# Optimization experiments

Hardware: AMD Instinct MI355X
Metric: run time of the kernel (lower is better)

## Reference

```python
import jax, jax.numpy as jnp
import numpy as np

B, NA, NB, E = 2, 256, 256, 512
H1, H2 = 300, 100


def setup_inputs() -> dict:
    key = jax.random.key(0)
    ks = jax.random.split(key, 16)

    def n(k, shape, scale=1.0):
        return jax.random.normal(k, shape, dtype=jnp.float32) * scale

    z = lambda shape: jnp.zeros(shape, jnp.float32)
    return {
        "action_embedding": n(ks[0], (B, E, NA)),
        "anchor_embedding": n(ks[1], (B, E, NB)),
        "action_points": n(ks[2], (B, 3, NA)),
        "anchor_points": n(ks[3], (B, 3, NB)),
        # pairwise MLP kernel params: 2E -> 300 -> 100 -> 1
        "mlp_W1": n(ks[4], (2 * E, H1), (2 * E) ** -0.5),
        "mlp_b1": z((H1,)),
        "mlp_W2": n(ks[5], (H1, H2), H1 ** -0.5),
        "mlp_b2": z((H2,)),
        "mlp_W3": n(ks[6], (H2, 1), H2 ** -0.5),
        "mlp_b3": z((1,)),
        # PointNet [512,64,64,64,128,512] (1x1 convs) + Conv1d(512,1,bias=False)
        "pn_W0": n(ks[7], (64, 512), 512 ** -0.5),
        "pn_b0": z((64,)),
        "pn_W1": n(ks[8], (64, 64), 64 ** -0.5),
        "pn_b1": z((64,)),
        "pn_W2": n(ks[9], (64, 64), 64 ** -0.5),
        "pn_b2": z((64,)),
        "pn_W3": n(ks[10], (128, 64), 64 ** -0.5),
        "pn_b3": z((128,)),
        "pn_W4": n(ks[11], (512, 128), 128 ** -0.5),
        "pn_b4": z((512,)),
        "head_W": n(ks[12], (1, 512), 512 ** -0.5),
    }


def reference(action_embedding, anchor_embedding, action_points, anchor_points,
              mlp_W1, mlp_b1, mlp_W2, mlp_b2, mlp_W3, mlp_b3,
              pn_W0, pn_b0, pn_W1, pn_b1, pn_W2, pn_b2, pn_W3, pn_b3,
              pn_W4, pn_b4, head_W):
    P_A = action_points.transpose(0, 2, 1)      # (B, NA, 3)
    P_B = anchor_points.transpose(0, 2, 1)      # (B, NB, 3)
    Phi_A = action_embedding.transpose(0, 2, 1)  # (B, NA, E)
    Phi_B = anchor_embedding.transpose(0, 2, 1)  # (B, NB, E)
    Ed = Phi_A.shape[-1]

    # --- symmetric pairwise MLP kernel: softplus((mlp(cat(a,b)) + mlp(cat(b,a))) / 2) ---
    # First Linear layer is split so the O(NA*NB*2E) concat is never materialized:
    # cat(a,b) @ W1 == a @ W1[:E] + b @ W1[E:]
    W1a, W1b = mlp_W1[:Ed], mlp_W1[Ed:]

    def mlp_tail(h):  # h: (B, NA, NB, H1) pre-activation of layer 1
        h = jax.nn.relu(h)
        h = jax.nn.relu(h @ mlp_W2 + mlp_b2)
        return (h @ mlp_W3 + mlp_b3)[..., 0]  # (B, NA, NB)

    hA_a = Phi_A @ W1a  # (B, NA, H1)
    hA_b = Phi_A @ W1b
    hB_a = Phi_B @ W1a  # (B, NB, H1)
    hB_b = Phi_B @ W1b
    v1 = mlp_tail(hA_a[:, :, None, :] + hB_b[:, None, :, :] + mlp_b1)  # mlp(cat(x1,x2))
    v2 = mlp_tail(hB_a[:, None, :, :] + hA_b[:, :, None, :] + mlp_b1)  # mlp(cat(x2,x1))
    R_est = jax.nn.softplus((v1 + v2) * 0.5)  # (B, NA, NB) estimated distances

    # --- weighted multilateration (estimate_p), vectorized over (B, NA) ---
    # Linearized LS: ||p||^2 - 2 q_k^T p = r_k^2 - ||q_k||^2; subtract weighted means
    # to eliminate ||p||^2, then solve 3x3 weighted normal equations per action point.
    w = jnp.ones(P_B.shape[:2], R_est.dtype)            # (B, NB) uniform weights (last_attn=False)
    wsum = w.sum(-1, keepdims=True)                      # (B, 1)
    qbar = (w[..., None] * P_B).sum(1) / wsum            # (B, 3)
    bvec = (P_B ** 2).sum(-1)[:, None, :] - R_est ** 2   # (B, NA, NB)
    bbar = (w[:, None, :] * bvec).sum(-1) / wsum         # (B, NA)
    Amat = 2.0 * (P_B - qbar[:, None, :])                # (B, NB, 3)
    yvec = bvec - bbar[..., None]                        # (B, NA, NB)
    M = jnp.einsum('bki,bk,bkj->bij', Amat, w, Amat)     # (B, 3, 3)
    rhs = jnp.einsum('bki,bk,bak->bai', Amat, w, yvec)   # (B, NA, 3)
    P_A_B_pred = jnp.linalg.solve(M[:, None], rhs[..., None])[..., 0]  # (B, NA, 3)

    flow = (P_A_B_pred - P_A).transpose(0, 2, 1)         # (B, 3, NA)

    # --- PointNet flow-weight head (1x1 convs + ReLU, final conv no bias) ---
    x = action_embedding                                  # (B, 512, NA)
    for Wc, bc in ((pn_W0, pn_b0), (pn_W1, pn_b1), (pn_W2, pn_b2),
                   (pn_W3, pn_b3), (pn_W4, pn_b4)):
        x = jax.nn.relu(jnp.einsum('oi,bin->bon', Wc, x) + bc[None, :, None])
    weight = jnp.einsum('oi,bin->bon', head_W, x)        # (B, 1, NA)

    full_flow = jnp.concatenate([flow, weight], axis=1)  # (B, 4, NA)
    return full_flow
```

## Files before the change

### kernel.cpp

```cpp
#include <hip/hip_runtime.h>
#include <hip/hip_bf16.h>
#include <hip/hip_fp16.h>

typedef float f32x4 __attribute__((ext_vector_type(4)));
typedef float f32x16 __attribute__((ext_vector_type(16)));
typedef short s16x8 __attribute__((ext_vector_type(8)));
typedef _Float16 f16x8 __attribute__((ext_vector_type(8)));

#define OFF_EMBT   0u
#define OFF_W1T    1048576u
#define OFF_W2TSW  1662976u
#define OFF_W0BF   1740800u
#define OFF_HA     1806336u
#define OFF_R2     3051520u
#define WS_TOTAL   3575808u

__device__ __forceinline__ int pack_bf2(float a, float b) {
  __hip_bfloat162 h = __float22bfloat162_rn(make_float2(a, b));
  int r; __builtin_memcpy(&r, &h, 4); return r;
}
__device__ __forceinline__ unsigned pack_f16_2(float a, float b) {
  __half2 h = __float22half2_rn(make_float2(a, b));
  unsigned r; __builtin_memcpy(&r, &h, 4); return r;
}
__device__ __forceinline__ unsigned short bf16u(float f) {
  __hip_bfloat16 h = __float2bfloat16(f);
  unsigned short u; __builtin_memcpy(&u, &h, 2); return u;
}
__device__ __forceinline__ s16x8 i4_to_s8(int a, int b, int c, int d) {
  union { int i[4]; s16x8 s; } u;
  u.i[0] = a; u.i[1] = b; u.i[2] = c; u.i[3] = d; return u.s;
}
template<int CTRL>
__device__ __forceinline__ float dpp_add(float x) {
  int xi; __builtin_memcpy(&xi, &x, 4);
  int yi = __builtin_amdgcn_update_dpp(0, xi, CTRL, 0xf, 0xf, true);
  float y; __builtin_memcpy(&y, &yi, 4);
  return x + y;
}
__device__ __forceinline__ float swz_xor16(float x) {
  int xi; __builtin_memcpy(&xi, &x, 4);
  int yi = __builtin_amdgcn_ds_swizzle(xi, 0x401f);
  float y; __builtin_memcpy(&y, &yi, 4);
  return y;
}

__global__ __launch_bounds__(256) void ka_prep(
    const float* __restrict__ act_emb, const float* __restrict__ anc_emb,
    const float* __restrict__ W1, const float* __restrict__ W2,
    const float* __restrict__ W0pn, char* __restrict__ ws)
{
  __hip_bfloat16* embT  = (__hip_bfloat16*)(ws + OFF_EMBT);
  __hip_bfloat16* W1T   = (__hip_bfloat16*)(ws + OFF_W1T);
  unsigned short* W2Tsw = (unsigned short*)(ws + OFF_W2TSW);
  unsigned short* W0bf  = (unsigned short*)(ws + OFF_W0BF);
  __shared__ float tile[64][65];
  int blk = blockIdx.x, t = threadIdx.x;
  if (blk < 128) {
    int b = blk >> 6, emb = (blk >> 5) & 1, ntile = (blk >> 3) & 3, etile = blk & 7;
    const float* src = emb ? anc_emb : act_emb;
    int e0 = etile * 64, n0 = ntile * 64;
    int rr = t >> 6, cc = t & 63;
    #pragma unroll
    for (int it2 = 0; it2 < 16; ++it2) {
      int e_l = rr * 16 + it2;
      tile[e_l][cc] = src[(size_t)(b * 512 + e0 + e_l) * 256 + n0 + cc];
    }
    __syncthreads();
    int n_l = t >> 2, eq = t & 3;
    unsigned int* dst = (unsigned int*)(embT + ((size_t)((b * 2 + emb) * 256 + n0 + n_l)) * 512 + e0 + eq * 16);
    #pragma unroll
    for (int kk = 0; kk < 8; ++kk)
      dst[kk] = (unsigned)pack_bf2(tile[eq * 16 + 2 * kk][n_l], tile[eq * 16 + 2 * kk + 1][n_l]);
  } else if (blk < 208) {
    int id = blk - 128;
    int half = id / 40; int rem = id % 40; int et = rem / 5; int ct = rem % 5;
    int e0 = et * 64, c0 = ct * 64;
    int rr = t >> 6, cc = t & 63;
    #pragma unroll
    for (int it2 = 0; it2 < 16; ++it2) {
      int e_l = rr * 16 + it2;
      int c = c0 + cc;
      tile[e_l][cc] = (c < 300) ? W1[(size_t)(half * 512 + e0 + e_l) * 300 + c] : 0.f;
    }
    __syncthreads();
    int c_l = t >> 2, eq = t & 3;
    if (c0 + c_l < 300) {
      unsigned int* dst = (unsigned int*)(W1T + ((size_t)(half * 300 + c0 + c_l)) * 512 + e0 + eq * 16);
      #pragma unroll
      for (int kk = 0; kk < 8; ++kk)
        dst[kk] = (unsigned)pack_bf2(tile[eq * 16 + 2 * kk][c_l], tile[eq * 16 + 2 * kk + 1][c_l]);
    }
  } else if (blk < 227) {
    int idx = (blk - 208) * 256 + t;
    int lane = idx & 63; int ntks = idx >> 6; int nt = ntks & 3; int ks = ntks >> 2;
    int n = nt * 32 + (lane & 31);
    int kb = ks * 16 + (lane >> 5) * 8;
    unsigned int q[4];
    #pragma unroll
    for (int jj = 0; jj < 4; ++jj) {
      int k0 = kb + jj * 2, k1 = kb + jj * 2 + 1;
      float f0 = (n < 100 && k0 < 300) ? W2[(size_t)k0 * 100 + n] : 0.f;
      float f1 = (n < 100 && k1 < 300) ? W2[(size_t)k1 * 100 + n] : 0.f;
      q[jj] = pack_f16_2(f0, f1);
    }
    ((uint4*)W2Tsw)[idx] = make_uint4(q[0], q[1], q[2], q[3]);
  } else if (blk < 243) {
    int idx = (blk - 227) * 256 + t;
    const float* s = W0pn + (size_t)idx * 8;
    ((uint4*)W0bf)[idx] = make_uint4(
        (unsigned)pack_bf2(s[0], s[1]), (unsigned)pack_bf2(s[2], s[3]),
        (unsigned)pack_bf2(s[4], s[5]), (unsigned)pack_bf2(s[6], s[7]));
  } else {
    int idx = (blk - 243) * 256 + t;
    _Float16* ha = (_Float16*)(ws + OFF_HA);
    #pragma unroll
    for (int rr = 0; rr < 2; ++rr) {
      int row = idx * 2 + rr;
      unsigned* p = (unsigned*)(ha + (size_t)row * 304 + 300);
      p[0] = 0u; p[1] = 0u;
    }
  }
}

template<int K, int NT>
__device__ __forceinline__ void pn_layer(unsigned short* xb, const float* __restrict__ W,
                                         const float* __restrict__ bias, int wv, int l, int g)
{
  constexpr int NN = NT / 4;
  f32x4 z = {0.f, 0.f, 0.f, 0.f};
  f32x4 acc[NN];
  #pragma unroll
  for (int nn = 0; nn < NN; ++nn) acc[nn] = z;
  #pragma unroll
  for (int nn = 0; nn < NN; ++nn) {
    int o = (wv + nn * 4) * 16 + l;
    const float* wr0 = W + (size_t)o * K;
    #pragma unroll
    for (int ks = 0; ks < K / 32; ++ks) {
      int koff = ks * 32 + g * 8;
      f32x4 wa = *(const f32x4*)(wr0 + koff);
      f32x4 wb = *(const f32x4*)(wr0 + koff + 4);
      s16x8 bfr = i4_to_s8(pack_bf2(wa.x, wa.y), pack_bf2(wa.z, wa.w),
                           pack_bf2(wb.x, wb.y), pack_bf2(wb.z, wb.w));
      s16x8 a0 = *(const s16x8*)(xb + (size_t)l * 520 + koff);
      acc[nn] = __builtin_amdgcn_mfma_f32_16x16x32_bf16(a0, bfr, acc[nn], 0, 0, 0);
    }
  }
  __syncthreads();
  #pragma unroll
  for (int nn = 0; nn < NN; ++nn) {
    int chan = (wv + nn * 4) * 16 + l;
    float bv = bias[chan];
    #pragma unroll
    for (int r = 0; r < 4; ++r)
      xb[(size_t)(g * 4 + r) * 520 + chan] = bf16u(fmaxf(acc[nn][r] + bv, 0.f));
  }
  __syncthreads();
}

__global__ __launch_bounds__(256) void k1_ha(
    const __hip_bfloat16* __restrict__ embT, const __hip_bfloat16* __restrict__ W1T,
    const float* __restrict__ b1, _Float16* __restrict__ ha_ws,
    const unsigned short* __restrict__ W0bf,
    const float* __restrict__ pnW1, const float* __restrict__ pnW2,
    const float* __restrict__ pnW3, const float* __restrict__ pnW4,
    const float* __restrict__ pnB0, const float* __restrict__ pnB1,
    const float* __restrict__ pnB2, const float* __restrict__ pnB3,
    const float* __restrict__ pnB4,
    const float* __restrict__ headW, float* __restrict__ out)
{
  __shared__ unsigned short xbuf[16 * 520];
  int blk = blockIdx.x, t = threadIdx.x;
  int wv = t >> 6, lane = t & 63, l = lane & 15, g = lane >> 4;
  if (blk < 320) {
    int b = blk / 160; int r = blk % 160; int emb = r / 80; r %= 80;
    int mch = r / 5; int nch = r % 5;
    int m0 = mch * 16;
    const unsigned short* Ap = (const unsigned short*)embT +
        ((size_t)((b * 2 + emb) * 256 + m0 + l)) * 512;
    const unsigned short* Wp = (const unsigned short*)W1T;
    f32x4 z = {0.f, 0.f, 0.f, 0.f};
    f32x4 acc[2] = {z, z};
    for (int ks = 0; ks < 16; ++ks) {
      int k0 = ks * 32 + g * 8;
      s16x8 af = *(const s16x8*)(Ap + k0);
      #pragma unroll
      for (int q = 0; q < 2; ++q) {
        int c = nch * 120 + (wv * 2 + q) * 16 + l;
        s16x8 bf = {0, 0, 0, 0, 0, 0, 0, 0};
        if (c < 600) bf = *(const s16x8*)(Wp + (size_t)c * 512 + k0);
        acc[q] = __builtin_amdgcn_mfma_f32_16x16x32_bf16(af, bf, acc[q], 0, 0, 0);
      }
    }
    #pragma unroll
    for (int q = 0; q < 2; ++q) {
      int cl = (wv * 2 + q) * 16 + l;
      int c = nch * 120 + cl;
      if (cl < 120 && c < 600) {
        int half = (c >= 300) ? 1 : 0;
        int cc = c - half * 300;
        float bias = (emb == 0) ? b1[cc] : 0.f;
        _Float16* Dp = ha_ws + ((size_t)((b * 4 + emb * 2 + half) * 256 + m0 + g * 4)) * 304 + cc;
        #pragma unroll
        for (int r2 = 0; r2 < 4; ++r2)
          Dp[(size_t)r2 * 304] = (_Float16)__float2half_rn(acc[q][r2] + bias);
      }
    }
  } else {
    int pn = blk - 320;
    int b_pn = pn >> 4, n0 = (pn & 15) * 16;
    unsigned short* xb = xbuf;
    {
      const unsigned short* A0 = (const unsigned short*)embT + ((size_t)(b_pn * 2 * 256 + n0)) * 512;
      f32x4 acc0 = {0.f, 0.f, 0.f, 0.f};
      int o = wv * 16 + l;
      const unsigned short* w0r = W0bf + (size_t)o * 512;
      #pragma unroll
      for (int ks = 0; ks < 16; ++ks) {
        int koff = ks * 32 + g * 8;
        s16x8 bfr = *(const s16x8*)(w0r + koff);
        s16x8 a0 = *(const s16x8*)(A0 + (size_t)l * 512 + koff);
        acc0 = __builtin_amdgcn_mfma_f32_16x16x32_bf16(a0, bfr, acc0, 0, 0, 0);
      }
      float bv = pnB0[o];
      #pragma unroll
      for (int r2 = 0; r2 < 4; ++r2)
        xb[(size_t)(g * 4 + r2) * 520 + o] = bf16u(fmaxf(acc0[r2] + bv, 0.f));
      __syncthreads();
    }
    pn_layer<64, 4>(xb, pnW1, pnB1, wv, l, g);
    pn_layer<64, 4>(xb, pnW2, pnB2, wv, l, g);
    pn_layer<64, 8>(xb, pnW3, pnB3, wv, l, g);
    pn_layer<128, 32>(xb, pnW4, pnB4, wv, l, g);
    {
      int p_l = t >> 4, os = t & 15;
      const unsigned short* row = xb + (size_t)p_l * 520 + os * 32;
      float s = 0.f;
      #pragma unroll
      for (int c = 0; c < 32; ++c) {
        unsigned int u = ((unsigned int)row[c]) << 16;
        float xv; __builtin_memcpy(&xv, &u, 4);
        s += xv * headW[os * 32 + c];
      }
      s += __shfl_xor(s, 1); s += __shfl_xor(s, 2);
      s += __shfl_xor(s, 4); s += __shfl_xor(s, 8);
      if (os == 0) out[(size_t)(b_pn * 4 + 3) * 256 + n0 + p_l] = s;
    }
  }
}

__global__ __launch_bounds__(512, 4) void k2_main(
    const _Float16* __restrict__ ha_ws, const unsigned short* __restrict__ W2Tsw,
    const float* __restrict__ b2g, const float* __restrict__ W3g, const float* __restrict__ b3g,
    float* __restrict__ R2)
{
  __shared__ int4 w2s[4864];
  __shared__ float ex[4][2][16];
  int blk = blockIdx.x, t = threadIdx.x;
  int wv = t >> 6, lane = t & 63, col = lane & 31, hi = lane >> 5;
  int jl = wv & 3, nh = wv >> 2;
  int u = blk; int b = u >> 8; u &= 255; int it = u >> 5; int jtp = u & 31;
  int i0 = it * 32;
  int j0 = jtp * 8 + jl;
  {
    const int4* w2g = (const int4*)W2Tsw;
    #pragma unroll
    for (int q = 0; q < 9; ++q) { int idx = t + q * 512; w2s[idx] = w2g[idx]; }
    { int idx = t + 9 * 512; if (idx < 4864) w2s[idx] = w2g[idx]; }
  }
  const _Float16* pA0 = ha_ws + ((size_t)((b * 4 + 0) * 256 + i0 + col)) * 304 + hi * 8;
  const _Float16* pA1 = ha_ws + ((size_t)((b * 4 + 1) * 256 + i0 + col)) * 304 + hi * 8;
  const _Float16* pB0 = ha_ws + ((size_t)((b * 4 + 3) * 256 + j0)) * 304 + hi * 8;
  const _Float16* pB1 = ha_ws + ((size_t)((b * 4 + 2) * 256 + j0)) * 304 + hi * 8;
  f16x8 a0c = *(const f16x8*)(pA0);
  f16x8 a1c = *(const f16x8*)(pA1);
  f16x8 b0c = *(const f16x8*)(pB0);
  f16x8 b1c = *(const f16x8*)(pB1);
  __syncthreads();

  const f16x8 zf = {0, 0, 0, 0, 0, 0, 0, 0};
  const int4* wbase = &w2s[nh * 128 + lane];
  f32x16 z16;
  #pragma unroll
  for (int q = 0; q < 16; ++q) z16[q] = 0.f;

  #pragma unroll 1
  for (int s = 0; s < 2; ++s) {
    f32x16 acc00 = z16, acc01 = z16, acc10 = z16, acc11 = z16;
    #pragma unroll 1
    for (int ks = 0; ks < 19; ++ks) {
      f16x8 a0n, a1n, b0n, b1n;
      if (ks < 18) {
        int ko = (ks + 1) * 16;
        a0n = *(const f16x8*)(pA0 + ko);
        a1n = *(const f16x8*)(pA1 + ko);
        b0n = *(const f16x8*)(pB0 + s * 1216 + ko);
        b1n = *(const f16x8*)(pB1 + s * 1216 + ko);
      } else if (s == 0) {
        a0n = *(const f16x8*)(pA0);
        a1n = *(const f16x8*)(pA1);
        b0n = *(const f16x8*)(pB0 + 1216);
        b1n = *(const f16x8*)(pB1 + 1216);
      } else {
        a0n = a0c; a1n = a1c; b0n = b0c; b1n = b1c;
      }
      f16x8 af0 = __builtin_elementwise_max(a0c + b0c, zf);
      f16x8 af1 = __builtin_elementwise_max(a1c + b1c, zf);
      const int4* wp = wbase + ks * 256;
      f16x8 bf0 = *(const f16x8*)(wp);
      f16x8 bf1 = *(const f16x8*)(wp + 64);
      acc00 = __builtin_amdgcn_mfma_f32_32x32x16_f16(af0, bf0, acc00, 0, 0, 0);
      acc01 = __builtin_amdgcn_mfma_f32_32x32x16_f16(af0, bf1, acc01, 0, 0, 0);
      acc10 = __builtin_amdgcn_mfma_f32_32x32x16_f16(af1, bf0, acc10, 0, 0, 0);
      acc11 = __builtin_amdgcn_mfma_f32_32x32x16_f16(af1, bf1, acc11, 0, 0, 0);
      a0c = a0n; a1c = a1n; b0c = b0n; b1c = b1n;
    }
    int j = j0 + s * 4;
    int n0 = nh * 64 + col, n1 = n0 + 32;
    float w3v0 = (n0 < 100) ? W3g[n0] : 0.f;
    float w3v1 = (n1 < 100) ? W3g[n1] : 0.f;
    float b2v0 = (n0 < 100) ? b2g[n0] : 0.f;
    float b2v1 = (n1 < 100) ? b2g[n1] : 0.f;
    float b3 = b3g[0];
    float mine = 0.f;
    #pragma unroll
    for (int r = 0; r < 16; ++r) {
      float x = fmaxf(acc00[r] + b2v0, 0.f) * w3v0 + fmaxf(acc01[r] + b2v1, 0.f) * w3v1
              + fmaxf(acc10[r] + b2v0, 0.f) * w3v0 + fmaxf(acc11[r] + b2v1, 0.f) * w3v1;
      x = dpp_add<0xB1>(x);
      x = dpp_add<0x4E>(x);
      x = dpp_add<0x141>(x);
      x = dpp_add<0x140>(x);
      x += swz_xor16(x);
      if (col == r) mine = x;
    }
    __syncthreads();
    if (nh == 1 && col < 16) ex[jl][hi][col] = mine;
    __syncthreads();
    if (nh == 0 && col < 16) {
      float tot = mine + ex[jl][hi][col];
      float S = 0.5f * tot + b3;
      float Rr = (S > 20.f) ? S : log1pf(expf(S));
      int il = (col & 3) + 8 * (col >> 2) + 4 * hi;
      R2[((size_t)(b * 256 + i0 + il)) * 256 + j] = Rr * Rr;
    }
  }
}

__device__ __forceinline__ float block_sum(float v, float* redbuf, int t) {
  #pragma unroll
  for (int m = 1; m < 64; m <<= 1) v += __shfl_xor(v, m);
  __syncthreads();
  if ((t & 63) == 0) redbuf[t >> 6] = v;
  __syncthreads();
  return redbuf[0] + redbuf[1] + redbuf[2] + redbuf[3];
}

__global__ __launch_bounds__(256) void k3_solve(
    const float* __restrict__ anc_pts, const float* __restrict__ act_pts,
    const float* __restrict__ R2, float* __restrict__ out)
{
  __shared__ float Ax[256], Ay[256], Az[256];
  __shared__ float redbuf[4];
  int blk = blockIdx.x, t = threadIdx.x;
  int b = blk >> 2, ic = blk & 3;
  int k = t;
  float px = anc_pts[(size_t)(b * 3 + 0) * 256 + k];
  float py = anc_pts[(size_t)(b * 3 + 1) * 256 + k];
  float pz = anc_pts[(size_t)(b * 3 + 2) * 256 + k];
  float qx = block_sum(px, redbuf, t) * (1.f / 256.f);
  float qy = block_sum(py, redbuf, t) * (1.f / 256.f);
  float qz = block_sum(pz, redbuf, t) * (1.f / 256.f);
  float ax = 2.f * (px - qx), ay = 2.f * (py - qy), az = 2.f * (pz - qz);
  float p2 = px * px + py * py + pz * pz;
  Ax[k] = ax; Ay[k] = ay; Az[k] = az;
  float mxx = block_sum(ax * ax, redbuf, t);
  float mxy = block_sum(ax * ay, redbuf, t);
  float mxz = block_sum(ax * az, redbuf, t);
  float myy = block_sum(ay * ay, redbuf, t);
  float myz = block_sum(ay * az, redbuf, t);
  float mzz = block_sum(az * az, redbuf, t);
  float c0x = block_sum(ax * p2, redbuf, t);
  float c0y = block_sum(ay * p2, redbuf, t);
  float c0z = block_sum(az * p2, redbuf, t);
  __syncthreads();
  float det = mxx * (myy * mzz - myz * myz) - mxy * (mxy * mzz - myz * mxz) + mxz * (mxy * myz - myy * mxz);
  float idet = 1.f / det;
  float i00 = (myy * mzz - myz * myz) * idet;
  float i01 = (mxz * myz - mxy * mzz) * idet;
  float i02 = (mxy * myz - mxz * myy) * idet;
  float i11 = (mxx * mzz - mxz * mxz) * idet;
  float i12 = (mxy * mxz - mxx * myz) * idet;
  float i22 = (mxx * myy - mxy * mxy) * idet;
  int il = t >> 2, ks = t & 3;
  int i = ic * 64 + il;
  const float* rrow = R2 + ((size_t)(b * 256 + i)) * 256;
  float r0 = 0.f, r1 = 0.f, r2 = 0.f;
  #pragma unroll
  for (int kk = 0; kk < 16; ++kk) {
    int kb = ks * 64 + kk * 4;
    f32x4 rv = *(const f32x4*)(rrow + kb);
    r0 += Ax[kb] * rv.x + Ax[kb + 1] * rv.y + Ax[kb + 2] * rv.z + Ax[kb + 3] * rv.w;
    r1 += Ay[kb] * rv.x + Ay[kb + 1] * rv.y + Ay[kb + 2] * rv.z + Ay[kb + 3] * rv.w;
    r2 += Az[kb] * rv.x + Az[kb + 1] * rv.y + Az[kb + 2] * rv.z + Az[kb + 3] * rv.w;
  }
  r0 += __shfl_xor(r0, 1); r0 += __shfl_xor(r0, 2);
  r1 += __shfl_xor(r1, 1); r1 += __shfl_xor(r1, 2);
  r2 += __shfl_xor(r2, 1); r2 += __shfl_xor(r2, 2);
  if (ks == 0) {
    float hx = c0x - r0, hy = c0y - r1, hz = c0z - r2;
    float x0 = i00 * hx + i01 * hy + i02 * hz;
    float x1 = i01 * hx + i11 * hy + i12 * hz;
    float x2 = i02 * hx + i12 * hy + i22 * hz;
    out[(size_t)(b * 4 + 0) * 256 + i] = x0 - act_pts[(size_t)(b * 3 + 0) * 256 + i];
    out[(size_t)(b * 4 + 1) * 256 + i] = x1 - act_pts[(size_t)(b * 3 + 1) * 256 + i];
    out[(size_t)(b * 4 + 2) * 256 + i] = x2 - act_pts[(size_t)(b * 3 + 2) * 256 + i];
  }
}

extern "C" void kernel_launch(void* const* d_in, const int* in_sizes, int n_in,
                              void* d_out, int out_size, void* d_ws, size_t ws_size,
                              hipStream_t stream)
{
  const float* act_emb = (const float*)d_in[0];
  const float* anc_emb = (const float*)d_in[1];
  const float* act_pts = (const float*)d_in[2];
  const float* anc_pts = (const float*)d_in[3];
  const float* W1  = (const float*)d_in[4];
  const float* b1  = (const float*)d_in[5];
  const float* W2  = (const float*)d_in[6];
  const float* b2  = (const float*)d_in[7];
  const float* W3  = (const float*)d_in[8];
  const float* b3  = (const float*)d_in[9];
  const float* pnW0 = (const float*)d_in[10];
  const float* pnB0 = (const float*)d_in[11];
  const float* pnW1 = (const float*)d_in[12];
  const float* pnB1 = (const float*)d_in[13];
  const float* pnW2 = (const float*)d_in[14];
  const float* pnB2 = (const float*)d_in[15];
  const float* pnW3 = (const float*)d_in[16];
  const float* pnB3 = (const float*)d_in[17];
  const float* pnW4 = (const float*)d_in[18];
  const float* pnB4 = (const float*)d_in[19];
  const float* headW = (const float*)d_in[20];
  char* ws = (char*)d_ws;
  __hip_bfloat16* embT  = (__hip_bfloat16*)(ws + OFF_EMBT);
  __hip_bfloat16* W1T   = (__hip_bfloat16*)(ws + OFF_W1T);
  unsigned short* W2Tsw = (unsigned short*)(ws + OFF_W2TSW);
  unsigned short* W0bf  = (unsigned short*)(ws + OFF_W0BF);
  _Float16* ha_ws = (_Float16*)(ws + OFF_HA);
  float* R2ws  = (float*)(ws + OFF_R2);
  float* outp  = (float*)d_out;

  ka_prep<<<247, 256, 0, stream>>>(act_emb, anc_emb, W1, W2, pnW0, ws);
  k1_ha<<<352, 256, 0, stream>>>(embT, W1T, b1, ha_ws, W0bf,
                                 pnW1, pnW2, pnW3, pnW4, pnB0, pnB1, pnB2, pnB3, pnB4,
                                 headW, outp);
  k2_main<<<512, 512, 0, stream>>>(ha_ws, W2Tsw, b2, W3, b3, R2ws);
  k3_solve<<<8, 256, 0, stream>>>(anc_pts, act_pts, R2ws, outp);
}
```

Measured before the change: 168.7 us.

## Store layer-1 activations in fragment-tiled layout and split waves by direction

k1 now writes the fp16 layer-1 activations into a tiled layout that matches the MFMA fragment shape, so each lane in k2 loads its fragment as one contiguous 16-byte vector. In k2, each wave now handles one direction (the ab or ba term) across all four N tiles, instead of both directions across half the N tiles. Activation loads are prefetched two K-steps ahead, and block indices are swizzled to spread work across XCDs. The intent is coalesced global loads, fewer A/B loads per MFMA and better latency hiding, at the cost of more LDS weight reads per step and tighter register pressure.

```diff
diff --git a/kernel.cpp b/kernel.cpp
--- a/kernel.cpp
+++ b/kernel.cpp
@@ -113,11 +113,13 @@
         (unsigned)pack_bf2(s[4], s[5]), (unsigned)pack_bf2(s[6], s[7]));
   } else {
     int idx = (blk - 243) * 256 + t;
-    _Float16* ha = (_Float16*)(ws + OFF_HA);
-    #pragma unroll
-    for (int rr = 0; rr < 2; ++rr) {
-      int row = idx * 2 + rr;
-      unsigned* p = (unsigned*)(ha + (size_t)row * 304 + 300);
+    _Float16* haf = (_Float16*)(ws + OFF_HA);
+    #pragma unroll
+    for (int u2 = 0; u2 < 2; ++u2) {
+      int unit = idx * 2 + u2;
+      int combo = unit >> 5, row = unit & 31;
+      size_t off = (((size_t)combo * 19 + 18) << 9) + (1 << 8) + (row << 3) + 4;
+      unsigned* p = (unsigned*)(haf + off);
       p[0] = 0u; p[1] = 0u;
     }
   }
@@ -161,7 +163,7 @@
 
 __global__ __launch_bounds__(256) void k1_ha(
     const __hip_bfloat16* __restrict__ embT, const __hip_bfloat16* __restrict__ W1T,
-    const float* __restrict__ b1, _Float16* __restrict__ ha_ws,
+    const float* __restrict__ b1, _Float16* __restrict__ ha_f,
     const unsigned short* __restrict__ W0bf,
     const float* __restrict__ pnW1, const float* __restrict__ pnW2,
     const float* __restrict__ pnW3, const float* __restrict__ pnW4,
@@ -201,10 +203,15 @@
         int half = (c >= 300) ? 1 : 0;
         int cc = c - half * 300;
         float bias = (emb == 0) ? b1[cc] : 0.f;
-        _Float16* Dp = ha_ws + ((size_t)((b * 4 + emb * 2 + half) * 256 + m0 + g * 4)) * 304 + cc;
+        int d = emb * 2 + half;
+        int ksf = cc >> 4, hi2 = (cc >> 3) & 1, e = cc & 7;
         #pragma unroll
-        for (int r2 = 0; r2 < 4; ++r2)
-          Dp[(size_t)r2 * 304] = (_Float16)__float2half_rn(acc[q][r2] + bias);
+        for (int r2 = 0; r2 < 4; ++r2) {
+          int i = m0 + g * 4 + r2;
+          size_t off = (((((size_t)(b * 4 + d)) * 8 + (i >> 5)) * 19 + ksf) << 9)
+                     + (hi2 << 8) + ((i & 31) << 3) + e;
+          ha_f[off] = (_Float16)__float2half_rn(acc[q][r2] + bias);
+        }
       }
     }
   } else {
@@ -251,15 +258,16 @@
 }
 
 __global__ __launch_bounds__(512, 4) void k2_main(
-    const _Float16* __restrict__ ha_ws, const unsigned short* __restrict__ W2Tsw,
+    const _Float16* __restrict__ haF, const unsigned short* __restrict__ W2Tsw,
     const float* __restrict__ b2g, const float* __restrict__ W3g, const float* __restrict__ b3g,
     float* __restrict__ R2)
 {
   __shared__ int4 w2s[4864];
   __shared__ float ex[4][2][16];
-  int blk = blockIdx.x, t = threadIdx.x;
+  int blkp = blockIdx.x, t = threadIdx.x;
+  int blk = (blkp & 7) * 64 + (blkp >> 3);
   int wv = t >> 6, lane = t & 63, col = lane & 31, hi = lane >> 5;
-  int jl = wv & 3, nh = wv >> 2;
+  int jl = wv & 3, dir = wv >> 2;
   int u = blk; int b = u >> 8; u &= 255; int it = u >> 5; int jtp = u & 31;
   int i0 = it * 32;
   int j0 = jtp * 8 + jl;
@@ -269,65 +277,59 @@
     for (int q = 0; q < 9; ++q) { int idx = t + q * 512; w2s[idx] = w2g[idx]; }
     { int idx = t + 9 * 512; if (idx < 4864) w2s[idx] = w2g[idx]; }
   }
-  const _Float16* pA0 = ha_ws + ((size_t)((b * 4 + 0) * 256 + i0 + col)) * 304 + hi * 8;
-  const _Float16* pA1 = ha_ws + ((size_t)((b * 4 + 1) * 256 + i0 + col)) * 304 + hi * 8;
-  const _Float16* pB0 = ha_ws + ((size_t)((b * 4 + 3) * 256 + j0)) * 304 + hi * 8;
-  const _Float16* pB1 = ha_ws + ((size_t)((b * 4 + 2) * 256 + j0)) * 304 + hi * 8;
-  f16x8 a0c = *(const f16x8*)(pA0);
-  f16x8 a1c = *(const f16x8*)(pA1);
-  f16x8 b0c = *(const f16x8*)(pB0);
-  f16x8 b1c = *(const f16x8*)(pB1);
+  const _Float16* pA = haF + ((((size_t)(b * 4 + dir)) * 8 + it) * 19) * 512 + lane * 8;
+  const _Float16* pB0 = haF + ((((size_t)(b * 4 + (3 - dir))) * 8 + (j0 >> 5)) * 19) * 512
+                        + (hi * 32 + (j0 & 31)) * 8;
   __syncthreads();
 
   const f16x8 zf = {0, 0, 0, 0, 0, 0, 0, 0};
-  const int4* wbase = &w2s[nh * 128 + lane];
   f32x16 z16;
   #pragma unroll
   for (int q = 0; q < 16; ++q) z16[q] = 0.f;
+  float b3 = b3g[0];
 
   #pragma unroll 1
   for (int s = 0; s < 2; ++s) {
-    f32x16 acc00 = z16, acc01 = z16, acc10 = z16, acc11 = z16;
-    #pragma unroll 1
+    const _Float16* pBs = pB0 + s * 32;
+    f16x8 aC = *(const f16x8*)(pA);
+    f16x8 aN = *(const f16x8*)(pA + 512);
+    f16x8 bC = *(const f16x8*)(pBs);
+    f16x8 bN = *(const f16x8*)(pBs + 512);
+    f32x16 acc0 = z16, acc1 = z16, acc2 = z16, acc3 = z16;
+    #pragma unroll 2
     for (int ks = 0; ks < 19; ++ks) {
-      f16x8 a0n, a1n, b0n, b1n;
-      if (ks < 18) {
-        int ko = (ks + 1) * 16;
-        a0n = *(const f16x8*)(pA0 + ko);
-        a1n = *(const f16x8*)(pA1 + ko);
-        b0n = *(const f16x8*)(pB0 + s * 1216 + ko);
-        b1n = *(const f16x8*)(pB1 + s * 1216 + ko);
-      } else if (s == 0) {
-        a0n = *(const f16x8*)(pA0);
-        a1n = *(const f16x8*)(pA1);
-        b0n = *(const f16x8*)(pB0 + 1216);
-        b1n = *(const f16x8*)(pB1 + 1216);
-      } else {
-        a0n = a0c; a1n = a1c; b0n = b0c; b1n = b1c;
-      }
-      f16x8 af0 = __builtin_elementwise_max(a0c + b0c, zf);
-      f16x8 af1 = __builtin_elementwise_max(a1c + b1c, zf);
-      const int4* wp = wbase + ks * 256;
+      f16x8 aN2, bN2;
+      if (ks <= 16) {
+        aN2 = *(const f16x8*)(pA + (ks + 2) * 512);
+        bN2 = *(const f16x8*)(pBs + (ks + 2) * 512);
+      } else { aN2 = aC; bN2 = bC; }
+      f16x8 af = __builtin_elementwise_max(aC + bC, zf);
+      const int4* wp = &w2s[ks * 256 + lane];
       f16x8 bf0 = *(const f16x8*)(wp);
       f16x8 bf1 = *(const f16x8*)(wp + 64);
-      acc00 = __builtin_amdgcn_mfma_f32_32x32x16_f16(af0, bf0, acc00, 0, 0, 0);
-      acc01 = __builtin_amdgcn_mfma_f32_32x32x16_f16(af0, bf1, acc01, 0, 0, 0);
-      acc10 = __builtin_amdgcn_mfma_f32_32x32x16_f16(af1, bf0, acc10, 0, 0, 0);
-      acc11 = __builtin_amdgcn_mfma_f32_32x32x16_f16(af1, bf1, acc11, 0, 0, 0);
-      a0c = a0n; a1c = a1n; b0c = b0n; b1c = b1n;
+      f16x8 bf2 = *(const f16x8*)(wp + 128);
+      f16x8 bf3 = *(const f16x8*)(wp + 192);
+      acc0 = __builtin_amdgcn_mfma_f32_32x32x16_f16(af, bf0, acc0, 0, 0, 0);
+      acc1 = __builtin_amdgcn_mfma_f32_32x32x16_f16(af, bf1, acc1, 0, 0, 0);
+      acc2 = __builtin_amdgcn_mfma_f32_32x32x16_f16(af, bf2, acc2, 0, 0, 0);
+      acc3 = __builtin_amdgcn_mfma_f32_32x32x16_f16(af, bf3, acc3, 0, 0, 0);
+      aC = aN; aN = aN2; bC = bN; bN = bN2;
     }
     int j = j0 + s * 4;
-    int n0 = nh * 64 + col, n1 = n0 + 32;
-    float w3v0 = (n0 < 100) ? W3g[n0] : 0.f;
-    float w3v1 = (n1 < 100) ? W3g[n1] : 0.f;
-    float b2v0 = (n0 < 100) ? b2g[n0] : 0.f;
-    float b2v1 = (n1 < 100) ? b2g[n1] : 0.f;
-    float b3 = b3g[0];
+    float w3v[4], b2v[4];
+    #pragma unroll
+    for (int nt = 0; nt < 4; ++nt) {
+      int n = nt * 32 + col;
+      w3v[nt] = (n < 100) ? W3g[n] : 0.f;
+      b2v[nt] = (n < 100) ? b2g[n] : 0.f;
+    }
     float mine = 0.f;
     #pragma unroll
     for (int r = 0; r < 16; ++r) {
-      float x = fmaxf(acc00[r] + b2v0, 0.f) * w3v0 + fmaxf(acc01[r] + b2v1, 0.f) * w3v1
-              + fmaxf(acc10[r] + b2v0, 0.f) * w3v0 + fmaxf(acc11[r] + b2v1, 0.f) * w3v1;
+      float x = fmaxf(acc0[r] + b2v[0], 0.f) * w3v[0]
+              + fmaxf(acc1[r] + b2v[1], 0.f) * w3v[1]
+              + fmaxf(acc2[r] + b2v[2], 0.f) * w3v[2]
+              + fmaxf(acc3[r] + b2v[3], 0.f) * w3v[3];
       x = dpp_add<0xB1>(x);
       x = dpp_add<0x4E>(x);
       x = dpp_add<0x141>(x);
@@ -336,9 +338,9 @@
       if (col == r) mine = x;
     }
     __syncthreads();
-    if (nh == 1 && col < 16) ex[jl][hi][col] = mine;
+    if (dir == 1 && col < 16) ex[jl][hi][col] = mine;
     __syncthreads();
-    if (nh == 0 && col < 16) {
+    if (dir == 0 && col < 16) {
       float tot = mine + ex[jl][hi][col];
       float S = 0.5f * tot + b3;
       float Rr = (S > 20.f) ? S : log1pf(expf(S));
@@ -449,14 +451,14 @@
   __hip_bfloat16* W1T   = (__hip_bfloat16*)(ws + OFF_W1T);
   unsigned short* W2Tsw = (unsigned short*)(ws + OFF_W2TSW);
   unsigned short* W0bf  = (unsigned short*)(ws + OFF_W0BF);
-  _Float16* ha_ws = (_Float16*)(ws + OFF_HA);
+  _Float16* ha_f = (_Float16*)(ws + OFF_HA);
   float* R2ws  = (float*)(ws + OFF_R2);
   float* outp  = (float*)d_out;
 
   ka_prep<<<247, 256, 0, stream>>>(act_emb, anc_emb, W1, W2, pnW0, ws);
-  k1_ha<<<352, 256, 0, stream>>>(embT, W1T, b1, ha_ws, W0bf,
+  k1_ha<<<352, 256, 0, stream>>>(embT, W1T, b1, ha_f, W0bf,
                                  pnW1, pnW2, pnW3, pnW4, pnB0, pnB1, pnB2, pnB3, pnB4,
                                  headW, outp);
-  k2_main<<<512, 512, 0, stream>>>(ha_ws, W2Tsw, b2, W3, b3, R2ws);
+  k2_main<<<512, 512, 0, stream>>>(ha_f, W2Tsw, b2, W3, b3, R2ws);
   k3_solve<<<8, 256, 0, stream>>>(anc_pts, act_pts, R2ws, outp);
 }
```

After: 170.8 us. No clear change (+1.3%).
